# Kernel tuning notes

Hardware: AMD Instinct MI355X
Metric: run time of the kernel (lower is better)

## Reference

```python
import jax, jax.numpy as jnp
import numpy as np

B, D, K = 8192, 256, 3
ALPHA, LAMBDA_NEG, GAMMA_SEMI = 0.7, 0.7, 0.7


def setup_inputs() -> dict:
    key = jax.random.key(0)
    k1, k2, k3 = jax.random.split(key, 3)
    text_embeddings = jax.random.normal(k1, (B, D), dtype=jnp.float32)
    image_embeddings = jax.random.normal(k2, (B, D), dtype=jnp.float32)
    # resolved pseudo-GT indices; -1 marks 'id not found in batch'
    semi_positive_indices = jax.random.randint(k3, (B, K), -1, B).astype(jnp.int32)
    return {
        "text_embeddings": text_embeddings,
        "image_embeddings": image_embeddings,
        "semi_positive_indices": semi_positive_indices,
    }


def _l2_normalize(x, eps=1e-12):
    n = jnp.sqrt(jnp.sum(x * x, axis=1, keepdims=True))
    return x / jnp.maximum(n, eps)


def reference(text_embeddings, image_embeddings, semi_positive_indices):
    t = _l2_normalize(text_embeddings)
    v = _l2_normalize(image_embeddings)
    sim = t @ v.T  # [B, B]
    b = sim.shape[0]

    rows = jnp.arange(b, dtype=semi_positive_indices.dtype)[:, None]  # [B,1]
    idx = semi_positive_indices  # [B,K]
    valid = (idx >= 0) & (idx != rows)  # exclude missing ids and the diagonal
    safe_idx = jnp.clip(idx, 0, b - 1)
    rows_b = jnp.broadcast_to(rows, idx.shape)
    semi_mask = jnp.zeros((b, b), dtype=bool).at[rows_b, safe_idx].max(valid)

    eye = jnp.eye(b, dtype=bool)
    diag = jnp.diagonal(sim)
    l_pos = jnp.sum((diag - 1.0) ** 2)

    semi_term = jnp.where(semi_mask, jnp.maximum(ALPHA - sim, 0.0), 0.0)
    l_semi_pos = jnp.sum(semi_term ** 2)

    neg_mask = ~(eye | semi_mask)
    neg_term = jnp.where(neg_mask, jnp.maximum(sim, 0.0), 0.0)
    l_neg = jnp.sum(neg_term ** 2)

    return l_pos + LAMBDA_NEG * l_neg + GAMMA_SEMI * l_semi_pos
```

## Files before the change

### kernel.cpp

```cpp
#include <hip/hip_runtime.h>

#define BDIM 8192
#define DDIM 256
#define NSLOTS 512

typedef __bf16 bf16x8 __attribute__((ext_vector_type(8)));
typedef float f32x4 __attribute__((ext_vector_type(4)));
typedef unsigned short u16x4 __attribute__((ext_vector_type(4)));

__device__ inline unsigned short f2bf(float f) {
  unsigned u = __float_as_uint(f);
  u += 0x7FFFu + ((u >> 16) & 1u);
  return (unsigned short)(u >> 16);
}
__device__ inline float bf2f(unsigned short h) {
  return __uint_as_float(((unsigned)h) << 16);
}

__device__ inline void gload_lds16(const void* g, void* l) {
  __builtin_amdgcn_global_load_lds(
      (const __attribute__((address_space(1))) void*)g,
      (__attribute__((address_space(3))) void*)l, 16, 0, 0);
}

__global__ __launch_bounds__(256) void norm_convert_kernel(
    const float* __restrict__ t, const float* __restrict__ v,
    unsigned short* __restrict__ tn, unsigned short* __restrict__ vn) {
  int wid = threadIdx.x >> 6, lane = threadIdx.x & 63;
  int row = blockIdx.x * 4 + wid;
  const float* src;
  unsigned short* dst;
  if (row < BDIM) {
    src = t + (size_t)row * DDIM;
    dst = tn + (size_t)row * DDIM;
  } else {
    int r = row - BDIM;
    src = v + (size_t)r * DDIM;
    dst = vn + (size_t)r * DDIM;
  }
  float4 x = reinterpret_cast<const float4*>(src)[lane];
  float ss = x.x * x.x + x.y * x.y + x.z * x.z + x.w * x.w;
  #pragma unroll
  for (int off = 1; off < 64; off <<= 1) ss += __shfl_xor(ss, off, 64);
  float sc = 1.0f / fmaxf(sqrtf(ss), 1e-12f);
  u16x4 w;
  w[0] = f2bf(x.x * sc); w[1] = f2bf(x.y * sc);
  w[2] = f2bf(x.z * sc); w[3] = f2bf(x.w * sc);
  reinterpret_cast<u16x4*>(dst)[lane] = w;
}

__global__ __launch_bounds__(256) void loss_kernel(
    const unsigned short* __restrict__ tn,
    const unsigned short* __restrict__ vn, float* __restrict__ slots) {
  __shared__ unsigned short As[128 * 64];
  __shared__ unsigned short Bs[128 * 64];
  __shared__ float rbuf[4];

  const int tid = threadIdx.x;
  const int lane = tid & 63;
  const int wid = tid >> 6;
  const int l15 = lane & 15;
  const int l4 = lane >> 4;

  const int flat = blockIdx.y * 64 + blockIdx.x;
  const int nb = (flat & 7) * 512 + (flat >> 3);
  const int rowBase = (nb >> 6) * 128;
  const int colBase = (nb & 63) * 128;

  const int srow = wid * 32 + (lane >> 3);
  const int scol = (((lane & 7) ^ (lane >> 3)) << 4) >> 1;
  const unsigned short* gA = tn + (size_t)(rowBase + srow) * DDIM + scol;
  const unsigned short* gB = vn + (size_t)(colBase + srow) * DDIM + scol;
  unsigned short* lA = As + wid * 2048;
  unsigned short* lB = Bs + wid * 2048;

  const int wr = (wid >> 1) * 64;
  const int wc = (wid & 1) * 64;

  f32x4 acc[4][4];
  #pragma unroll
  for (int i = 0; i < 4; ++i)
    #pragma unroll
    for (int j = 0; j < 4; ++j) acc[i][j] = (f32x4)(0.0f);

  for (int ks = 0; ks < 4; ++ks) {
    if (ks) __syncthreads();
    #pragma unroll
    for (int q = 0; q < 4; ++q) {
      gload_lds16(gA + (size_t)q * 8 * DDIM + ks * 64, lA + q * 512);
      gload_lds16(gB + (size_t)q * 8 * DDIM + ks * 64, lB + q * 512);
    }
    __syncthreads();
    #pragma unroll
    for (int kk = 0; kk < 2; ++kk) {
      bf16x8 af[4], bfr[4];
      const int cb = ((kk * 64 + l4 * 16) ^ ((l15 & 7) << 4)) >> 1;
      #pragma unroll
      for (int m = 0; m < 4; ++m) {
        int row = wr + m * 16 + l15;
        af[m] = *reinterpret_cast<const bf16x8*>(&As[row * 64 + cb]);
      }
      #pragma unroll
      for (int n = 0; n < 4; ++n) {
        int row = wc + n * 16 + l15;
        bfr[n] = *reinterpret_cast<const bf16x8*>(&Bs[row * 64 + cb]);
      }
      #pragma unroll
      for (int m = 0; m < 4; ++m)
        #pragma unroll
        for (int n = 0; n < 4; ++n)
          acc[m][n] = __builtin_amdgcn_mfma_f32_16x16x32_bf16(
              af[m], bfr[n], acc[m][n], 0, 0, 0);
    }
  }

  float lsum = 0.0f;
  #pragma unroll
  for (int m = 0; m < 4; ++m)
    #pragma unroll
    for (int n = 0; n < 4; ++n)
      #pragma unroll
      for (int r = 0; r < 4; ++r) {
        float u = fmaxf(acc[m][n][r], 0.0f);
        lsum = fmaf(u, u, lsum);
      }
  lsum *= 0.7f;
  #pragma unroll
  for (int off = 1; off < 64; off <<= 1) lsum += __shfl_xor(lsum, off, 64);
  if (lane == 0) rbuf[wid] = lsum;
  __syncthreads();
  if (tid == 0)
    atomicAdd(&slots[flat & (NSLOTS - 1)],
              rbuf[0] + rbuf[1] + rbuf[2] + rbuf[3]);
}

__global__ __launch_bounds__(256) void corr_kernel(
    const unsigned short* __restrict__ tn,
    const unsigned short* __restrict__ vn, const int* __restrict__ sidx,
    float* __restrict__ slots) {
  int wid = threadIdx.x >> 6, lane = threadIdx.x & 63;
  int i = blockIdx.x * 4 + wid;

  u16x4 ta = reinterpret_cast<const u16x4*>(tn + (size_t)i * DDIM)[lane];
  float t0 = bf2f(ta[0]), t1 = bf2f(ta[1]), t2 = bf2f(ta[2]), t3 = bf2f(ta[3]);

  int j0 = sidx[(size_t)i * 3 + 0];
  int j1 = sidx[(size_t)i * 3 + 1];
  int j2 = sidx[(size_t)i * 3 + 2];
  bool v0 = (j0 >= 0) & (j0 < BDIM) & (j0 != i);
  bool v1 = (j1 >= 0) & (j1 < BDIM) & (j1 != i) & !(v0 & (j1 == j0));
  bool v2 = (j2 >= 0) & (j2 < BDIM) & (j2 != i) & !(v0 & (j2 == j0)) &
            !(v1 & (j2 == j1));

  float corr = 0.0f;
  {
    u16x4 va = reinterpret_cast<const u16x4*>(vn + (size_t)i * DDIM)[lane];
    float d = t0 * bf2f(va[0]) + t1 * bf2f(va[1]) + t2 * bf2f(va[2]) +
              t3 * bf2f(va[3]);
    #pragma unroll
    for (int off = 1; off < 64; off <<= 1) d += __shfl_xor(d, off, 64);
    float u = fmaxf(d, 0.0f);
    corr += (d - 1.0f) * (d - 1.0f) - 0.7f * u * u;
  }
  int jj[3] = {j0, j1, j2};
  bool vv[3] = {v0, v1, v2};
  #pragma unroll
  for (int k = 0; k < 3; ++k) {
    int j = vv[k] ? jj[k] : i;
    u16x4 va = reinterpret_cast<const u16x4*>(vn + (size_t)j * DDIM)[lane];
    float d = t0 * bf2f(va[0]) + t1 * bf2f(va[1]) + t2 * bf2f(va[2]) +
              t3 * bf2f(va[3]);
    #pragma unroll
    for (int off = 1; off < 64; off <<= 1) d += __shfl_xor(d, off, 64);
    if (vv[k]) {
      float up = fmaxf(0.7f - d, 0.0f);
      float un = fmaxf(d, 0.0f);
      corr += 0.7f * (up * up - un * un);
    }
  }
  if (lane == 0) atomicAdd(&slots[i & (NSLOTS - 1)], corr);
}

__global__ __launch_bounds__(256) void reduce_kernel(
    const float* __restrict__ slots, float* __restrict__ out) {
  __shared__ float rb[4];
  int tid = threadIdx.x;
  float s = slots[tid] + slots[tid + 256];
  #pragma unroll
  for (int off = 1; off < 64; off <<= 1) s += __shfl_xor(s, off, 64);
  if ((tid & 63) == 0) rb[tid >> 6] = s;
  __syncthreads();
  if (tid == 0) out[0] = rb[0] + rb[1] + rb[2] + rb[3];
}

extern "C" void kernel_launch(void* const* d_in, const int* in_sizes, int n_in,
                              void* d_out, int out_size, void* d_ws,
                              size_t ws_size, hipStream_t stream) {
  const float* t = (const float*)d_in[0];
  const float* v = (const float*)d_in[1];
  const int* sidx = (const int*)d_in[2];
  float* out = (float*)d_out;
  float* slots = (float*)d_ws;
  unsigned short* tn = (unsigned short*)((char*)d_ws + 4096);
  unsigned short* vn = tn + (size_t)BDIM * DDIM;

  hipMemsetAsync(slots, 0, NSLOTS * sizeof(float), stream);
  norm_convert_kernel<<<4096, 256, 0, stream>>>(t, v, tn, vn);
  dim3 grid(64, 64);
  loss_kernel<<<grid, 256, 0, stream>>>(tn, vn, slots);
  corr_kernel<<<2048, 256, 0, stream>>>(tn, vn, sidx, slots);
  reduce_kernel<<<1, 256, 0, stream>>>(slots, out);
}
```

Before: 64.19 us.

## Use 256x256 tiles with double-buffered LDS prefetch in loss GEMM

The loss GEMM moves from 128x128 tiles with 256 threads to 256x256 tiles with 512 threads (8 waves, each computing 128x64). The LDS is double-buffered so global-to-LDS loads for the next K slice are issued while the current slice is computed. This uses explicit vmcnt waits, raw barriers and s_setprio around the MFMA blocks. It aims to raise arithmetic intensity and hide load latency, at the cost of 128KB of LDS per block and only 1024 blocks, which lowers occupancy and tail balance.

```diff
diff --git a/kernel.cpp b/kernel.cpp
--- a/kernel.cpp
+++ b/kernel.cpp
@@ -7,6 +7,15 @@
 typedef __bf16 bf16x8 __attribute__((ext_vector_type(8)));
 typedef float f32x4 __attribute__((ext_vector_type(4)));
 typedef unsigned short u16x4 __attribute__((ext_vector_type(4)));
+
+#define MEMF() asm volatile("" ::: "memory")
+#define BARR()                       \
+  do {                               \
+    MEMF();                          \
+    __builtin_amdgcn_s_barrier();    \
+    MEMF();                          \
+  } while (0)
+#define VMW(n) asm volatile("s_waitcnt vmcnt(" #n ")" ::: "memory")
 
 __device__ inline unsigned short f2bf(float f) {
   unsigned u = __float_as_uint(f);
@@ -49,74 +58,112 @@
   reinterpret_cast<u16x4*>(dst)[lane] = w;
 }
 
-__global__ __launch_bounds__(256) void loss_kernel(
+__global__ __launch_bounds__(512) void loss_kernel(
     const unsigned short* __restrict__ tn,
     const unsigned short* __restrict__ vn, float* __restrict__ slots) {
-  __shared__ unsigned short As[128 * 64];
-  __shared__ unsigned short Bs[128 * 64];
-  __shared__ float rbuf[4];
+  __shared__ unsigned short Asb[2][16384];
+  __shared__ unsigned short Bsb[2][16384];
+  __shared__ float rbuf[8];
 
   const int tid = threadIdx.x;
   const int lane = tid & 63;
   const int wid = tid >> 6;
   const int l15 = lane & 15;
   const int l4 = lane >> 4;
-
-  const int flat = blockIdx.y * 64 + blockIdx.x;
-  const int nb = (flat & 7) * 512 + (flat >> 3);
-  const int rowBase = (nb >> 6) * 128;
-  const int colBase = (nb & 63) * 128;
-
-  const int srow = wid * 32 + (lane >> 3);
-  const int scol = (((lane & 7) ^ (lane >> 3)) << 4) >> 1;
-  const unsigned short* gA = tn + (size_t)(rowBase + srow) * DDIM + scol;
-  const unsigned short* gB = vn + (size_t)(colBase + srow) * DDIM + scol;
-  unsigned short* lA = As + wid * 2048;
-  unsigned short* lB = Bs + wid * 2048;
-
-  const int wr = (wid >> 1) * 64;
-  const int wc = (wid & 1) * 64;
-
-  f32x4 acc[4][4];
-  #pragma unroll
-  for (int i = 0; i < 4; ++i)
+  const int wm = wid >> 2;
+  const int wn = wid & 3;
+
+  const int flat = blockIdx.x;
+  const int nb = (flat & 7) * 128 + (flat >> 3);
+  const int rowBase = (nb >> 5) * 256;
+  const int colBase = (nb & 31) * 256;
+
+  const int sg = (tid & 7) ^ ((tid >> 3) & 7);
+  const unsigned short* gAsrc =
+      tn + (size_t)(rowBase + (tid >> 3)) * DDIM + sg * 8;
+  const unsigned short* gBsrc =
+      vn + (size_t)(colBase + (tid >> 3)) * DDIM + sg * 8;
+  const int ldsStage = wid * 512;
+
+  auto stA = [&](int ob, int rg, int kt) {
+    gload_lds16(gAsrc + (size_t)rg * 64 * DDIM + kt * 64,
+                &Asb[ob][rg * 4096 + ldsStage]);
+  };
+  auto stB = [&](int ob, int rg, int kt) {
+    gload_lds16(gBsrc + (size_t)rg * 64 * DDIM + kt * 64,
+                &Bsb[ob][rg * 4096 + ldsStage]);
+  };
+
+  stB(0, 0, 0); stB(0, 1, 0); stB(0, 2, 0); stB(0, 3, 0);
+  stA(0, 0, 0); stA(0, 2, 0);
+  stA(0, 1, 0); stA(0, 3, 0);
+  VMW(2);
+  BARR();
+
+  f32x4 acc[8][4];
+  #pragma unroll
+  for (int i = 0; i < 8; ++i)
     #pragma unroll
     for (int j = 0; j < 4; ++j) acc[i][j] = (f32x4)(0.0f);
 
-  for (int ks = 0; ks < 4; ++ks) {
-    if (ks) __syncthreads();
+  #pragma unroll
+  for (int t = 0; t < 4; ++t) {
+    const int cur = t & 1, ob = cur ^ 1, kt = t + 1;
     #pragma unroll
     for (int q = 0; q < 4; ++q) {
-      gload_lds16(gA + (size_t)q * 8 * DDIM + ks * 64, lA + q * 512);
-      gload_lds16(gB + (size_t)q * 8 * DDIM + ks * 64, lB + q * 512);
+      const int mh = q >> 1, nh = q & 1;
+      bf16x8 af[4][2], bv[2][2];
+      #pragma unroll
+      for (int mm = 0; mm < 4; ++mm) {
+        const int row = wm * 128 + (mh * 4 + mm) * 16 + l15;
+        #pragma unroll
+        for (int kk = 0; kk < 2; ++kk) {
+          const int gg = (kk * 4 + l4) ^ (l15 & 7);
+          af[mm][kk] =
+              *reinterpret_cast<const bf16x8*>(&Asb[cur][row * 64 + gg * 8]);
+        }
+      }
+      #pragma unroll
+      for (int nn = 0; nn < 2; ++nn) {
+        const int row = wn * 64 + (nh * 2 + nn) * 16 + l15;
+        #pragma unroll
+        for (int kk = 0; kk < 2; ++kk) {
+          const int gg = (kk * 4 + l4) ^ (l15 & 7);
+          bv[nn][kk] =
+              *reinterpret_cast<const bf16x8*>(&Bsb[cur][row * 64 + gg * 8]);
+        }
+      }
+      if (t < 3) {
+        if (q == 0)      { stB(ob, 0, kt); stB(ob, 1, kt); }
+        else if (q == 1) { stB(ob, 2, kt); stB(ob, 3, kt); }
+        else if (q == 2) { stA(ob, 0, kt); stA(ob, 2, kt); }
+        else             { stA(ob, 1, kt); stA(ob, 3, kt); }
+      }
+      if (q == 1) {
+        if (t < 3) VMW(4); else VMW(0);
+      }
+      if (q == 3 && t < 3) VMW(2);
+      BARR();
+      asm volatile("s_waitcnt lgkmcnt(0)" ::: "memory");
+      __builtin_amdgcn_s_setprio(1);
+      #pragma unroll
+      for (int mm = 0; mm < 4; ++mm)
+        #pragma unroll
+        for (int nn = 0; nn < 2; ++nn)
+          #pragma unroll
+          for (int kk = 0; kk < 2; ++kk)
+            acc[mh * 4 + mm][nh * 2 + nn] =
+                __builtin_amdgcn_mfma_f32_16x16x32_bf16(
+                    af[mm][kk], bv[nn][kk], acc[mh * 4 + mm][nh * 2 + nn], 0,
+                    0, 0);
+      __builtin_amdgcn_s_setprio(0);
+      BARR();
     }
-    __syncthreads();
-    #pragma unroll
-    for (int kk = 0; kk < 2; ++kk) {
-      bf16x8 af[4], bfr[4];
-      const int cb = ((kk * 64 + l4 * 16) ^ ((l15 & 7) << 4)) >> 1;
-      #pragma unroll
-      for (int m = 0; m < 4; ++m) {
-        int row = wr + m * 16 + l15;
-        af[m] = *reinterpret_cast<const bf16x8*>(&As[row * 64 + cb]);
-      }
-      #pragma unroll
-      for (int n = 0; n < 4; ++n) {
-        int row = wc + n * 16 + l15;
-        bfr[n] = *reinterpret_cast<const bf16x8*>(&Bs[row * 64 + cb]);
-      }
-      #pragma unroll
-      for (int m = 0; m < 4; ++m)
-        #pragma unroll
-        for (int n = 0; n < 4; ++n)
-          acc[m][n] = __builtin_amdgcn_mfma_f32_16x16x32_bf16(
-              af[m], bfr[n], acc[m][n], 0, 0, 0);
-    }
   }
 
   float lsum = 0.0f;
   #pragma unroll
-  for (int m = 0; m < 4; ++m)
+  for (int m = 0; m < 8; ++m)
     #pragma unroll
     for (int n = 0; n < 4; ++n)
       #pragma unroll
@@ -129,9 +176,12 @@
   for (int off = 1; off < 64; off <<= 1) lsum += __shfl_xor(lsum, off, 64);
   if (lane == 0) rbuf[wid] = lsum;
   __syncthreads();
-  if (tid == 0)
-    atomicAdd(&slots[flat & (NSLOTS - 1)],
-              rbuf[0] + rbuf[1] + rbuf[2] + rbuf[3]);
+  if (tid == 0) {
+    float s = 0.0f;
+    #pragma unroll
+    for (int w = 0; w < 8; ++w) s += rbuf[w];
+    atomicAdd(&slots[flat & (NSLOTS - 1)], s);
+  }
 }
 
 __global__ __launch_bounds__(256) void corr_kernel(
@@ -206,8 +256,7 @@
 
   hipMemsetAsync(slots, 0, NSLOTS * sizeof(float), stream);
   norm_convert_kernel<<<4096, 256, 0, stream>>>(t, v, tn, vn);
-  dim3 grid(64, 64);
-  loss_kernel<<<grid, 256, 0, stream>>>(tn, vn, slots);
+  loss_kernel<<<1024, 512, 0, stream>>>(tn, vn, slots);
   corr_kernel<<<2048, 256, 0, stream>>>(tn, vn, sidx, slots);
   reduce_kernel<<<1, 256, 0, stream>>>(slots, out);
 }
```

Measured after the change: 69.81 us. 1.09x slower.
